# Optimization experiments

Measured on AMD Instinct MI355X. Metric: run time of the kernel, lower is better.

## Reference

```python
import jax, jax.numpy as jnp
import numpy as np
import math

NUM_HEADS = 8


def _dwconv(x, w, b, pad):
    # depthwise conv: x (B,C,H,W), w (C,1,k,k)
    c = x.shape[1]
    y = jax.lax.conv_general_dilated(
        x, w, window_strides=(1, 1), padding=[(pad, pad), (pad, pad)],
        feature_group_count=c, dimension_numbers=("NCHW", "OIHW", "NCHW"))
    return y + b[None, :, None, None]


def _conv(x, w, b, pad):
    y = jax.lax.conv_general_dilated(
        x, w, window_strides=(1, 1), padding=[(pad, pad), (pad, pad)],
        dimension_numbers=("NCHW", "OIHW", "NCHW"))
    return y + b[None, :, None, None]


def setup_inputs() -> dict:
    key = jax.random.key(0)
    ks = jax.random.split(key, 6)
    B, C, H, W = 8, 128, 128, 128
    x = jax.random.normal(ks[0], (B, C, H, W), dtype=jnp.float32)
    wq = jax.random.normal(ks[1], (C, 1, 9, 9), dtype=jnp.float32) * 0.05
    wk = jax.random.normal(ks[2], (C, 1, 9, 9), dtype=jnp.float32) * 0.05
    wv = jax.random.normal(ks[3], (C, 1, 9, 9), dtype=jnp.float32) * 0.05
    wo = jax.random.normal(ks[4], (C, C, 3, 3), dtype=jnp.float32) * 0.02
    bq = jnp.zeros((C,), jnp.float32)
    bk = jnp.zeros((C,), jnp.float32)
    bv = jnp.zeros((C,), jnp.float32)
    bo = jnp.zeros((C,), jnp.float32)
    return {"x": x, "wq": wq, "bq": bq, "wk": wk, "bk": bk,
            "wv": wv, "bv": bv, "wo": wo, "bo": bo}


def reference(x, wq, bq, wk, bk, wv, bv, wo, bo):
    b, c, h, w = x.shape
    hds = NUM_HEADS
    d = (h * w) // hds  # spatial dim split across heads
    q = _dwconv(x, wq, bq, 4).reshape(b, c, hds, d).transpose(0, 2, 1, 3)  # (b,hds,c,d)
    k = _dwconv(x, wk, bk, 4).reshape(b, c, hds, d).transpose(0, 2, 3, 1)  # (b,hds,d,c)
    v = _dwconv(x, wv, bv, 4).reshape(b, c, hds, d).transpose(0, 2, 1, 3)  # (b,hds,c,d)
    # channel attention: C x C scores per head, fp32 softmax
    qk = jnp.einsum("bhcd,bhde->bhce", q.astype(jnp.float32), k.astype(jnp.float32)) / math.sqrt(h * w)
    a = jnp.einsum("bhce,bhed->bhcd", jax.nn.softmax(qk, axis=-1), v.astype(jnp.float32))
    a = a.transpose(0, 2, 1, 3).reshape(b, c, h, w)
    return _conv(a, wo, bo, 1)
```

## Files before the change

### kernel.cpp

```cpp
#include <hip/hip_runtime.h>

#define BATCH 8
#define CH 128
#define HH 128
#define WW 128
#define HWSZ 16384
#define NHEADS 8
#define DHEAD 2048

typedef short bf16x8 __attribute__((ext_vector_type(8)));
typedef short bf16x4v __attribute__((ext_vector_type(4)));
typedef float f32x4 __attribute__((ext_vector_type(4)));
typedef float f32x2 __attribute__((ext_vector_type(2)));
typedef _Float16 f16x8 __attribute__((ext_vector_type(8)));
typedef _Float16 f16x4 __attribute__((ext_vector_type(4)));

static __device__ inline unsigned short f2bf(float f) {
    unsigned u = __builtin_bit_cast(unsigned, f);
    u += 0x7fff + ((u >> 16) & 1);
    return (unsigned short)(u >> 16);
}

__global__ __launch_bounds__(256) void toeplitz_prep_kernel(
    const float* __restrict__ wq, const float* __restrict__ wk,
    const float* __restrict__ wv, _Float16* __restrict__ Tp)
{
    const int g = blockIdx.x * 256 + threadIdx.x;
    const int c    = g / 1728;
    const int rem  = g - c * 1728;
    const int m    = rem >> 6;
    const int lane = rem & 63;
    const int conv = m / 9;
    const int dy   = m - conv * 9;
    const float* w = (conv == 0) ? wq : ((conv == 1) ? wk : wv);
    const int j    = lane & 15;
    const int kb   = (lane >> 4) << 3;
    f16x8 h;
    #pragma unroll
    for (int e = 0; e < 8; ++e) {
        const int d = kb + e - j;
        h[e] = (d >= 0 && d <= 8) ? (_Float16)w[c * 81 + dy * 9 + d]
                                  : (_Float16)0.f;
    }
    *(f16x8*)&Tp[(size_t)g * 8] = h;
}

__global__ __launch_bounds__(256) void dwconv_qkv_mfma_kernel(
    const float* __restrict__ x,
    const float* __restrict__ bq, const float* __restrict__ bk,
    const float* __restrict__ bv,
    const _Float16* __restrict__ Tp,
    unsigned short* __restrict__ Qb, unsigned short* __restrict__ Kb,
    unsigned short* __restrict__ Vb)
{
    const int bc = blockIdx.x;
    const int b  = bc >> 7;
    const int c  = bc & (CH - 1);

    __shared__ _Float16 img[136][144];

    const int tid  = threadIdx.x;
    const int wave = tid >> 6;
    const int lane = tid & 63;
    const int lx   = lane & 15;
    const int qd   = lane >> 4;

    f16x8 Btp[27];
    const _Float16* tp = Tp + (size_t)c * 13824 + (size_t)lane * 8;
    #pragma unroll
    for (int m = 0; m < 27; ++m)
        Btp[m] = *(const f16x8*)(tp + (size_t)m * 512);

    {
        f16x8 z = {0, 0, 0, 0, 0, 0, 0, 0};
        _Float16* flat = &img[0][0];
        for (int i = tid; i < 2448; i += 256)
            *(f16x8*)&flat[i * 8] = z;
    }
    __syncthreads();
    const float* xp = x + (size_t)bc * HWSZ;
    for (int i = tid; i < 4096; i += 256) {
        const float4 v = *(const float4*)&xp[i * 4];
        const int y  = i >> 5;
        const int xc = (i & 31) << 2;
        f16x4 h = {(_Float16)v.x, (_Float16)v.y, (_Float16)v.z, (_Float16)v.w};
        *(f16x4*)&img[y + 4][xc + 4] = h;
    }
    __syncthreads();

    const float bqv = bq[c], bkv = bk[c], bvv = bv[c];

    #pragma unroll 1
    for (int t = 0; t < 8; ++t) {
        const int sg = t * 4 + wave;
        const int yg = sg >> 2;
        const int y0 = yg << 4;
        const int x0 = (sg & 3) << 5;

        f32x4 aq0 = {bqv, bqv, bqv, bqv}, aq1 = aq0;
        f32x4 ak0 = {bkv, bkv, bkv, bkv}, ak1 = ak0;
        f32x4 av0 = {bvv, bvv, bvv, bvv}, av1 = av0;

        const _Float16* rp = &img[y0 + lx][x0 + (qd << 3)];
        #pragma unroll
        for (int dy = 0; dy < 9; ++dy) {
            const f16x8 a0 = *(const f16x8*)rp;
            const f16x8 a1 = *(const f16x8*)(rp + 16);
            rp += 144;
            aq0 = __builtin_amdgcn_mfma_f32_16x16x32_f16(a0, Btp[dy],      aq0, 0, 0, 0);
            aq1 = __builtin_amdgcn_mfma_f32_16x16x32_f16(a1, Btp[dy],      aq1, 0, 0, 0);
            ak0 = __builtin_amdgcn_mfma_f32_16x16x32_f16(a0, Btp[9 + dy],  ak0, 0, 0, 0);
            ak1 = __builtin_amdgcn_mfma_f32_16x16x32_f16(a1, Btp[9 + dy],  ak1, 0, 0, 0);
            av0 = __builtin_amdgcn_mfma_f32_16x16x32_f16(a0, Btp[18 + dy], av0, 0, 0, 0);
            av1 = __builtin_amdgcn_mfma_f32_16x16x32_f16(a1, Btp[18 + dy], av1, 0, 0, 0);
        }

        const size_t base = ((size_t)(b * 8 + yg) * CH + c) * DHEAD
                          + (size_t)(qd << 2) * WW + x0 + lx;
        #pragma unroll
        for (int r = 0; r < 4; ++r) {
            Qb[base + r * WW]      = f2bf(aq0[r]);
            Qb[base + r * WW + 16] = f2bf(aq1[r]);
            Kb[base + r * WW]      = f2bf(ak0[r]);
            Kb[base + r * WW + 16] = f2bf(ak1[r]);
            Vb[base + r * WW]      = f2bf(av0[r]);
            Vb[base + r * WW + 16] = f2bf(av1[r]);
        }
    }
}

__global__ __launch_bounds__(256) void qk_mfma_kernel(
    const unsigned short* __restrict__ Qb, const unsigned short* __restrict__ Kb,
    float* __restrict__ Spart)
{
    const int blk   = blockIdx.x;
    const int split = blk & 7;
    const int bh    = blk >> 3;
    const int t0    = split * 256;

    __shared__ unsigned short Qs[128][72];
    __shared__ unsigned short Ks[128][72];

    const int tid  = threadIdx.x;
    const int wave = tid >> 6;
    const int lane = tid & 63;
    const int lx   = lane & 15;
    const int qd   = lane >> 4;
    const int m0   = (wave & 1) * 64;
    const int n0   = (wave >> 1) * 64;

    f32x4 acc[4][4];
    #pragma unroll
    for (int mi = 0; mi < 4; ++mi)
        #pragma unroll
        for (int ni = 0; ni < 4; ++ni) acc[mi][ni] = (f32x4){0.f, 0.f, 0.f, 0.f};

    const unsigned short* Qp = Qb + (size_t)bh * CH * DHEAD;
    const unsigned short* Kp = Kb + (size_t)bh * CH * DHEAD;

    #pragma unroll 1
    for (int tc = 0; tc < 256; tc += 64) {
        __syncthreads();
        for (int i = tid; i < 1024; i += 256) {
            const int r  = i >> 3;
            const int cl = (i & 7) << 3;
            *(bf16x8*)&Qs[r][cl] = *(const bf16x8*)&Qp[(size_t)r * DHEAD + t0 + tc + cl];
            *(bf16x8*)&Ks[r][cl] = *(const bf16x8*)&Kp[(size_t)r * DHEAD + t0 + tc + cl];
        }
        __syncthreads();
        #pragma unroll
        for (int ki = 0; ki < 2; ++ki) {
            const int kc = ki * 32 + qd * 8;
            bf16x8 a[4], bv[4];
            #pragma unroll
            for (int mi = 0; mi < 4; ++mi)
                a[mi] = *(const bf16x8*)&Qs[m0 + mi * 16 + lx][kc];
            #pragma unroll
            for (int ni = 0; ni < 4; ++ni)
                bv[ni] = *(const bf16x8*)&Ks[n0 + ni * 16 + lx][kc];
            #pragma unroll
            for (int mi = 0; mi < 4; ++mi)
                #pragma unroll
                for (int ni = 0; ni < 4; ++ni)
                    acc[mi][ni] = __builtin_amdgcn_mfma_f32_16x16x32_bf16(
                        a[mi], bv[ni], acc[mi][ni], 0, 0, 0);
        }
    }
    float* Sp = Spart + ((size_t)split * 64 + bh) * (CH * CH);
    #pragma unroll
    for (int mi = 0; mi < 4; ++mi)
        #pragma unroll
        for (int r = 0; r < 4; ++r) {
            const int c = m0 + mi * 16 + qd * 4 + r;
            #pragma unroll
            for (int ni = 0; ni < 4; ++ni)
                Sp[c * CH + n0 + ni * 16 + lx] = acc[mi][ni][r];
        }
}

__global__ __launch_bounds__(256) void softmax_kernel(
    const float* __restrict__ Spart, unsigned short* __restrict__ Pb)
{
    const int row  = blockIdx.x * 4 + (threadIdx.x >> 6);
    const int lane = threadIdx.x & 63;
    float v0 = 0.f, v1 = 0.f;
    #pragma unroll
    for (int s = 0; s < 8; ++s) {
        const float* Sp = Spart + (size_t)s * 64 * CH * CH + (size_t)row * CH;
        v0 += Sp[lane];
        v1 += Sp[lane + 64];
    }
    v0 *= 0.0078125f; v1 *= 0.0078125f;
    float m = fmaxf(v0, v1);
    #pragma unroll
    for (int off = 32; off > 0; off >>= 1) m = fmaxf(m, __shfl_down(m, off));
    m = __shfl(m, 0);
    const float e0 = __expf(v0 - m);
    const float e1 = __expf(v1 - m);
    float s = e0 + e1;
    #pragma unroll
    for (int off = 32; off > 0; off >>= 1) s += __shfl_down(s, off);
    s = __shfl(s, 0);
    const float inv = 1.f / s;
    Pb[(size_t)row * CH + lane]      = f2bf(e0 * inv);
    Pb[(size_t)row * CH + lane + 64] = f2bf(e1 * inv);
}

__global__ __launch_bounds__(256) void pv_mfma_kernel(
    const unsigned short* __restrict__ Pb, const unsigned short* __restrict__ Vb,
    unsigned short* __restrict__ At)
{
    const int blk = blockIdx.x;
    const int t0  = (blk & 15) << 7;
    const int bh  = blk >> 4;

    __shared__ __align__(16) char smem[69632];
    unsigned short (*Ps)[136] = (unsigned short(*)[136])smem;
    unsigned short (*Vs)[136] = (unsigned short(*)[136])(smem + 34816);
    float (*So)[132] = (float(*)[132])smem;

    const int tid  = threadIdx.x;
    const int wave = tid >> 6;
    const int lane = tid & 63;
    const int lx   = lane & 15;
    const int qd   = lane >> 4;
    const int m0   = (wave & 1) * 64;
    const int n0   = (wave >> 1) * 64;

    const unsigned short* Pp = Pb + (size_t)bh * CH * CH;
    const unsigned short* Vp = Vb + (size_t)bh * CH * DHEAD;

    for (int i = tid; i < 2048; i += 256) {
        const int r  = i >> 4;
        const int cl = (i & 15) << 3;
        *(bf16x8*)&Ps[r][cl] = *(const bf16x8*)&Pp[(size_t)r * CH + cl];
    }
    for (int i = tid; i < 2048; i += 256) {
        const int e   = i & 127;
        const int tc8 = (i >> 7) << 3;
        const bf16x8 vv = *(const bf16x8*)&Vp[(size_t)e * DHEAD + t0 + tc8];
        #pragma unroll
        for (int j = 0; j < 8; ++j) Vs[tc8 + j][e] = (unsigned short)vv[j];
    }
    __syncthreads();

    f32x4 acc[4][4];
    #pragma unroll
    for (int mi = 0; mi < 4; ++mi)
        #pragma unroll
        for (int ni = 0; ni < 4; ++ni) acc[mi][ni] = (f32x4){0.f, 0.f, 0.f, 0.f};

    #pragma unroll
    for (int ki = 0; ki < 4; ++ki) {
        const int kc = ki * 32 + qd * 8;
        bf16x8 a[4], bv[4];
        #pragma unroll
        for (int mi = 0; mi < 4; ++mi)
            a[mi] = *(const bf16x8*)&Ps[m0 + mi * 16 + lx][kc];
        #pragma unroll
        for (int ni = 0; ni < 4; ++ni)
            bv[ni] = *(const bf16x8*)&Vs[n0 + ni * 16 + lx][kc];
        #pragma unroll
        for (int mi = 0; mi < 4; ++mi)
            #pragma unroll
            for (int ni = 0; ni < 4; ++ni)
                acc[mi][ni] = __builtin_amdgcn_mfma_f32_16x16x32_bf16(
                    a[mi], bv[ni], acc[mi][ni], 0, 0, 0);
    }

    __syncthreads();
    #pragma unroll
    for (int mi = 0; mi < 4; ++mi)
        #pragma unroll
        for (int ni = 0; ni < 4; ++ni)
            #pragma unroll
            for (int r = 0; r < 4; ++r)
                So[n0 + ni * 16 + lx][m0 + mi * 16 + qd * 4 + r] = acc[mi][ni][r];
    __syncthreads();

    const int t  = tid >> 1;
    const int ch = (tid & 1) * 64;
    const size_t orow = (((size_t)(bh >> 3) * HWSZ) + (size_t)(bh & 7) * DHEAD + t0 + t) * CH + ch;
    #pragma unroll
    for (int j = 0; j < 8; ++j) {
        const float4 f0 = *(const float4*)&So[t][ch + j * 8];
        const float4 f1 = *(const float4*)&So[t][ch + j * 8 + 4];
        bf16x8 h;
        h[0] = (short)f2bf(f0.x); h[1] = (short)f2bf(f0.y);
        h[2] = (short)f2bf(f0.z); h[3] = (short)f2bf(f0.w);
        h[4] = (short)f2bf(f1.x); h[5] = (short)f2bf(f1.y);
        h[6] = (short)f2bf(f1.z); h[7] = (short)f2bf(f1.w);
        *(bf16x8*)&At[orow + j * 8] = h;
    }
}

__global__ __launch_bounds__(256) void wprep_kernel(
    const float* __restrict__ wo, unsigned short* __restrict__ Wt)
{
    const int i = blockIdx.x * 256 + threadIdx.x;
    const int tap = i >> 14;
    const int rem = i & 16383;
    const int co  = rem >> 7;
    const int ci  = rem & 127;
    Wt[i] = f2bf(wo[(size_t)(co * CH + ci) * 9 + tap]);
}

__global__ __launch_bounds__(512, 2) void conv3x3_mfma_kernel(
    const unsigned short* __restrict__ At, const unsigned short* __restrict__ Wt,
    const float* __restrict__ bo, float* __restrict__ out)
{
    __shared__ __align__(16) char smem[149504];

    const int w    = ((blockIdx.x & 7) << 6) | (blockIdx.x >> 3);
    const int yp   = w & 63;
    const int b    = w >> 6;
    const int y0   = yp << 1;

    const int tid  = threadIdx.x;
    const int wave = tid >> 6;
    const int lane = tid & 63;
    const int lx   = lane & 15;
    const int qd   = lane >> 4;
    const int m0   = (wave & 1) << 6;
    const int n0   = (wave >> 1) << 6;
    const int rsel = n0 >> 7;
    const int xb   = n0 & 64;

    const int j0 = tid, j1 = tid + 512;
    const int co0 = j0 >> 3, cu0 = j0 & 7;
    const int co1 = j1 >> 3, cu1 = j1 & 7;
    const unsigned swo0 = (unsigned)((co0 * 128 + cu0 * 16) ^ ((co0 & 7) << 4)) + 133120u;
    const unsigned swo1 = (unsigned)((co1 * 128 + cu1 * 16) ^ ((co1 & 7) << 4)) + 133120u;

    float4 nwa = *(const float4*)&Wt[(size_t)co0 * 128 + cu0 * 8];
    float4 nwb = *(const float4*)&Wt[(size_t)co1 * 128 + cu1 * 8];

    const size_t abase = (size_t)b * HWSZ * CH;
    if (tid < 128) {
        const int r  = tid >> 5;
        const int cu = tid & 31;
        const int xp = (cu & 16) ? 129 : 0;
        const int u  = cu & 15;
        const unsigned off = (unsigned)(r * 33280 + xp * 256 + u * 16) ^ (((unsigned)xp & 7u) << 4);
        *(float4*)(smem + off) = make_float4(0.f, 0.f, 0.f, 0.f);
    }
    for (int i = tid; i < 8192; i += 512) {
        const int r   = i >> 11;
        const int rem = i & 2047;
        const int xx  = rem >> 4;
        const int u   = rem & 15;
        const int gy  = y0 - 1 + r;
        float4 v = make_float4(0.f, 0.f, 0.f, 0.f);
        if ((unsigned)gy < HH)
            v = *(const float4*)&At[abase + (size_t)gy * WW * CH + xx * CH + u * 8];
        const int xp = xx + 1;
        const unsigned off = (unsigned)(r * 33280 + xp * 256 + u * 16) ^ (((unsigned)xp & 7u) << 4);
        *(float4*)(smem + off) = v;
    }
    *(float4*)(smem + swo0) = nwa;
    *(float4*)(smem + swo1) = nwb;
    nwa = *(const float4*)&Wt[(size_t)co0 * 128 + 64 + cu0 * 8];
    nwb = *(const float4*)&Wt[(size_t)co1 * 128 + 64 + cu1 * 8];

    f32x4 acc[4][4];
    #pragma unroll
    for (int mi = 0; mi < 4; ++mi) {
        f32x4 bv;
        #pragma unroll
        for (int r = 0; r < 4; ++r) bv[r] = bo[m0 + mi * 16 + qd * 4 + r];
        #pragma unroll
        for (int ni = 0; ni < 4; ++ni) acc[mi][ni] = bv;
    }

    __syncthreads();

    #pragma unroll 1
    for (int s = 0; s < 18; ++s) {
        const int tap = s >> 1;
        const int dy  = (tap * 11) >> 5;
        const int txc = tap - dy * 3;
        const int kh  = s & 1;
        const int ra  = rsel + dy;

        #pragma unroll
        for (int ks = 0; ks < 2; ++ks) {
            const int wkb = ks * 64 + qd * 16;
            const int akb = kh * 128 + ks * 64 + qd * 16;
            bf16x8 a[4], bfr[4];
            #pragma unroll
            for (int mi = 0; mi < 4; ++mi) {
                const int co = m0 + mi * 16 + lx;
                a[mi] = *(const bf16x8*)(smem + 133120u +
                        (unsigned)((co * 128 + wkb) ^ ((co & 7) << 4)));
            }
            #pragma unroll
            for (int ni = 0; ni < 4; ++ni) {
                const int xp = xb + ni * 16 + lx + txc;
                const unsigned off = (unsigned)(ra * 33280 + xp * 256 + akb)
                                   ^ (((unsigned)xp & 7u) << 4);
                bfr[ni] = *(const bf16x8*)(smem + off);
            }
            #pragma unroll
            for (int mi = 0; mi < 4; ++mi)
                #pragma unroll
                for (int ni = 0; ni < 4; ++ni)
                    acc[mi][ni] = __builtin_amdgcn_mfma_f32_16x16x32_bf16(
                        a[mi], bfr[ni], acc[mi][ni], 0, 0, 0);
        }
        __syncthreads();
        if (s < 17) {
            *(float4*)(smem + swo0) = nwa;
            *(float4*)(smem + swo1) = nwb;
            if (s < 16) {
                const int s2 = s + 2;
                const size_t gb = (size_t)(s2 >> 1) * 16384 + (s2 & 1) * 64;
                nwa = *(const float4*)&Wt[gb + co0 * 128 + cu0 * 8];
                nwb = *(const float4*)&Wt[gb + co1 * 128 + cu1 * 8];
            }
            __syncthreads();
        }
    }

    const int gy = y0 + rsel;
    const size_t obase = (size_t)b * CH * HWSZ + (size_t)gy * WW + xb;
    #pragma unroll
    for (int mi = 0; mi < 4; ++mi) {
        #pragma unroll
        for (int r = 0; r < 4; ++r) {
            const int co = m0 + mi * 16 + qd * 4 + r;
            float* orow = out + obase + (size_t)co * HWSZ;
            #pragma unroll
            for (int ni = 0; ni < 4; ++ni)
                orow[ni * 16 + lx] = acc[mi][ni][r];
        }
    }
}

extern "C" void kernel_launch(void* const* d_in, const int* in_sizes, int n_in,
                              void* d_out, int out_size, void* d_ws, size_t ws_size,
                              hipStream_t stream)
{
    const float* x  = (const float*)d_in[0];
    const float* wq = (const float*)d_in[1];
    const float* bq = (const float*)d_in[2];
    const float* wk = (const float*)d_in[3];
    const float* bk = (const float*)d_in[4];
    const float* wv = (const float*)d_in[5];
    const float* bv = (const float*)d_in[6];
    const float* wo = (const float*)d_in[7];
    const float* bo = (const float*)d_in[8];

    char* ws = (char*)d_ws;
    unsigned short* Qb    = (unsigned short*)(ws);
    unsigned short* Kb    = (unsigned short*)(ws + (size_t)33554432);
    unsigned short* Vb    = (unsigned short*)(ws + (size_t)67108864);
    float*          Spart = (float*)        (ws + (size_t)100663296);
    unsigned short* Pb    = (unsigned short*)(ws + (size_t)134217728);
    unsigned short* At    = (unsigned short*)(ws + (size_t)136314880);
    unsigned short* Wt    = (unsigned short*)(ws + (size_t)169869312);
    _Float16*       Tp    = (_Float16*)      (ws + (size_t)100663296);

    toeplitz_prep_kernel<<<864, 256, 0, stream>>>(wq, wk, wv, Tp);
    dwconv_qkv_mfma_kernel<<<BATCH * CH, 256, 0, stream>>>(x, bq, bk, bv, Tp, Qb, Kb, Vb);
    wprep_kernel<<<576, 256, 0, stream>>>(wo, Wt);
    qk_mfma_kernel<<<64 * 8, 256, 0, stream>>>(Qb, Kb, Spart);
    softmax_kernel<<<2048, 256, 0, stream>>>(Spart, Pb);
    pv_mfma_kernel<<<64 * 16, 256, 0, stream>>>(Pb, Vb, At);
    conv3x3_mfma_kernel<<<BATCH * 64, 512, 0, stream>>>(At, Wt, bo, (float*)d_out);
}
```

Before: 268.9 us.

## Fuse QK and softmax, vectorize dwconv stores, double-buffer conv weights

Swaps the MFMA operand order in the depthwise conv so each lane holds four consecutive x outputs, which allows 8-byte vector stores in place of scalar bf16 stores. Replaces the split-K QK kernel plus separate softmax with one kernel: each block computes 32 full score rows over all of d and runs the softmax in shared memory. This drops the fp32 partial-score round trip and one launch, at the cost of fewer blocks (256) and a serial loop over d. The conv3x3 kernel double-buffers the weight tiles to remove one barrier per step and handles padding by zeroing operands in registers instead of keeping halo columns in shared memory, using a larger LDS allocation.

```diff
diff --git a/kernel.cpp b/kernel.cpp
--- a/kernel.cpp
+++ b/kernel.cpp
@@ -107,123 +107,157 @@
             const f16x8 a0 = *(const f16x8*)rp;
             const f16x8 a1 = *(const f16x8*)(rp + 16);
             rp += 144;
-            aq0 = __builtin_amdgcn_mfma_f32_16x16x32_f16(a0, Btp[dy],      aq0, 0, 0, 0);
-            aq1 = __builtin_amdgcn_mfma_f32_16x16x32_f16(a1, Btp[dy],      aq1, 0, 0, 0);
-            ak0 = __builtin_amdgcn_mfma_f32_16x16x32_f16(a0, Btp[9 + dy],  ak0, 0, 0, 0);
-            ak1 = __builtin_amdgcn_mfma_f32_16x16x32_f16(a1, Btp[9 + dy],  ak1, 0, 0, 0);
-            av0 = __builtin_amdgcn_mfma_f32_16x16x32_f16(a0, Btp[18 + dy], av0, 0, 0, 0);
-            av1 = __builtin_amdgcn_mfma_f32_16x16x32_f16(a1, Btp[18 + dy], av1, 0, 0, 0);
+            aq0 = __builtin_amdgcn_mfma_f32_16x16x32_f16(Btp[dy],      a0, aq0, 0, 0, 0);
+            aq1 = __builtin_amdgcn_mfma_f32_16x16x32_f16(Btp[dy],      a1, aq1, 0, 0, 0);
+            ak0 = __builtin_amdgcn_mfma_f32_16x16x32_f16(Btp[9 + dy],  a0, ak0, 0, 0, 0);
+            ak1 = __builtin_amdgcn_mfma_f32_16x16x32_f16(Btp[9 + dy],  a1, ak1, 0, 0, 0);
+            av0 = __builtin_amdgcn_mfma_f32_16x16x32_f16(Btp[18 + dy], a0, av0, 0, 0, 0);
+            av1 = __builtin_amdgcn_mfma_f32_16x16x32_f16(Btp[18 + dy], a1, av1, 0, 0, 0);
         }
 
         const size_t base = ((size_t)(b * 8 + yg) * CH + c) * DHEAD
-                          + (size_t)(qd << 2) * WW + x0 + lx;
-        #pragma unroll
-        for (int r = 0; r < 4; ++r) {
-            Qb[base + r * WW]      = f2bf(aq0[r]);
-            Qb[base + r * WW + 16] = f2bf(aq1[r]);
-            Kb[base + r * WW]      = f2bf(ak0[r]);
-            Kb[base + r * WW + 16] = f2bf(ak1[r]);
-            Vb[base + r * WW]      = f2bf(av0[r]);
-            Vb[base + r * WW + 16] = f2bf(av1[r]);
-        }
-    }
-}
-
-__global__ __launch_bounds__(256) void qk_mfma_kernel(
+                          + (size_t)lx * WW + x0 + (qd << 2);
+        bf16x4v h;
+        h[0] = (short)f2bf(aq0[0]); h[1] = (short)f2bf(aq0[1]);
+        h[2] = (short)f2bf(aq0[2]); h[3] = (short)f2bf(aq0[3]);
+        *(bf16x4v*)&Qb[base] = h;
+        h[0] = (short)f2bf(aq1[0]); h[1] = (short)f2bf(aq1[1]);
+        h[2] = (short)f2bf(aq1[2]); h[3] = (short)f2bf(aq1[3]);
+        *(bf16x4v*)&Qb[base + 16] = h;
+        h[0] = (short)f2bf(ak0[0]); h[1] = (short)f2bf(ak0[1]);
+        h[2] = (short)f2bf(ak0[2]); h[3] = (short)f2bf(ak0[3]);
+        *(bf16x4v*)&Kb[base] = h;
+        h[0] = (short)f2bf(ak1[0]); h[1] = (short)f2bf(ak1[1]);
+        h[2] = (short)f2bf(ak1[2]); h[3] = (short)f2bf(ak1[3]);
+        *(bf16x4v*)&Kb[base + 16] = h;
+        h[0] = (short)f2bf(av0[0]); h[1] = (short)f2bf(av0[1]);
+        h[2] = (short)f2bf(av0[2]); h[3] = (short)f2bf(av0[3]);
+        *(bf16x4v*)&Vb[base] = h;
+        h[0] = (short)f2bf(av1[0]); h[1] = (short)f2bf(av1[1]);
+        h[2] = (short)f2bf(av1[2]); h[3] = (short)f2bf(av1[3]);
+        *(bf16x4v*)&Vb[base + 16] = h;
+    }
+}
+
+__global__ __launch_bounds__(256) void qks_kernel(
     const unsigned short* __restrict__ Qb, const unsigned short* __restrict__ Kb,
-    float* __restrict__ Spart)
-{
-    const int blk   = blockIdx.x;
-    const int split = blk & 7;
-    const int bh    = blk >> 3;
-    const int t0    = split * 256;
-
-    __shared__ unsigned short Qs[128][72];
-    __shared__ unsigned short Ks[128][72];
+    unsigned short* __restrict__ Pb)
+{
+    const int blk = ((blockIdx.x & 7) << 5) | (blockIdx.x >> 3);
+    const int bh  = blk >> 2;
+    const int c0  = (blk & 3) << 5;
+
+    __shared__ __align__(16) char smem[41216];
 
     const int tid  = threadIdx.x;
     const int wave = tid >> 6;
     const int lane = tid & 63;
     const int lx   = lane & 15;
     const int qd   = lane >> 4;
-    const int m0   = (wave & 1) * 64;
-    const int n0   = (wave >> 1) * 64;
-
-    f32x4 acc[4][4];
-    #pragma unroll
-    for (int mi = 0; mi < 4; ++mi)
-        #pragma unroll
-        for (int ni = 0; ni < 4; ++ni) acc[mi][ni] = (f32x4){0.f, 0.f, 0.f, 0.f};
-
-    const unsigned short* Qp = Qb + (size_t)bh * CH * DHEAD;
+    const int n0   = wave << 5;
+
+    f32x4 acc[2][2];
+    #pragma unroll
+    for (int mi = 0; mi < 2; ++mi)
+        #pragma unroll
+        for (int ni = 0; ni < 2; ++ni) acc[mi][ni] = (f32x4){0.f, 0.f, 0.f, 0.f};
+
+    const unsigned short* Qp = Qb + ((size_t)bh * CH + c0) * DHEAD;
     const unsigned short* Kp = Kb + (size_t)bh * CH * DHEAD;
 
     #pragma unroll 1
-    for (int tc = 0; tc < 256; tc += 64) {
+    for (int chk = 0; chk < 16; ++chk) {
+        const int t0 = chk << 7;
         __syncthreads();
-        for (int i = tid; i < 1024; i += 256) {
-            const int r  = i >> 3;
-            const int cl = (i & 7) << 3;
-            *(bf16x8*)&Qs[r][cl] = *(const bf16x8*)&Qp[(size_t)r * DHEAD + t0 + tc + cl];
-            *(bf16x8*)&Ks[r][cl] = *(const bf16x8*)&Kp[(size_t)r * DHEAD + t0 + tc + cl];
+        for (int i = tid; i < 512; i += 256) {
+            const int r = i >> 4, u = i & 15;
+            const bf16x8 v = *(const bf16x8*)&Qp[(size_t)r * DHEAD + t0 + u * 8];
+            const unsigned off = (unsigned)((r << 8) + (u << 4)) ^ (((unsigned)r & 7u) << 4);
+            *(bf16x8*)(smem + off) = v;
+        }
+        for (int i = tid; i < 2048; i += 256) {
+            const int r = i >> 4, u = i & 15;
+            const bf16x8 v = *(const bf16x8*)&Kp[(size_t)r * DHEAD + t0 + u * 8];
+            const unsigned off = 8192u + ((unsigned)((r << 8) + (u << 4)) ^ (((unsigned)r & 7u) << 4));
+            *(bf16x8*)(smem + off) = v;
         }
         __syncthreads();
         #pragma unroll
-        for (int ki = 0; ki < 2; ++ki) {
+        for (int ki = 0; ki < 4; ++ki) {
             const int kc = ki * 32 + qd * 8;
-            bf16x8 a[4], bv[4];
-            #pragma unroll
-            for (int mi = 0; mi < 4; ++mi)
-                a[mi] = *(const bf16x8*)&Qs[m0 + mi * 16 + lx][kc];
-            #pragma unroll
-            for (int ni = 0; ni < 4; ++ni)
-                bv[ni] = *(const bf16x8*)&Ks[n0 + ni * 16 + lx][kc];
-            #pragma unroll
-            for (int mi = 0; mi < 4; ++mi)
+            bf16x8 a[2], bv[2];
+            #pragma unroll
+            for (int mi = 0; mi < 2; ++mi) {
+                const int r = mi * 16 + lx;
+                a[mi] = *(const bf16x8*)(smem +
+                        ((unsigned)((r << 8) + (kc << 1)) ^ (((unsigned)r & 7u) << 4)));
+            }
+            #pragma unroll
+            for (int ni = 0; ni < 2; ++ni) {
+                const int r = n0 + ni * 16 + lx;
+                bv[ni] = *(const bf16x8*)(smem + 8192u +
+                        ((unsigned)((r << 8) + (kc << 1)) ^ (((unsigned)r & 7u) << 4)));
+            }
+            #pragma unroll
+            for (int mi = 0; mi < 2; ++mi)
                 #pragma unroll
-                for (int ni = 0; ni < 4; ++ni)
+                for (int ni = 0; ni < 2; ++ni)
                     acc[mi][ni] = __builtin_amdgcn_mfma_f32_16x16x32_bf16(
                         a[mi], bv[ni], acc[mi][ni], 0, 0, 0);
         }
     }
-    float* Sp = Spart + ((size_t)split * 64 + bh) * (CH * CH);
-    #pragma unroll
-    for (int mi = 0; mi < 4; ++mi)
-        #pragma unroll
-        for (int r = 0; r < 4; ++r) {
-            const int c = m0 + mi * 16 + qd * 4 + r;
-            #pragma unroll
-            for (int ni = 0; ni < 4; ++ni)
-                Sp[c * CH + n0 + ni * 16 + lx] = acc[mi][ni][r];
-        }
-}
-
-__global__ __launch_bounds__(256) void softmax_kernel(
-    const float* __restrict__ Spart, unsigned short* __restrict__ Pb)
-{
-    const int row  = blockIdx.x * 4 + (threadIdx.x >> 6);
-    const int lane = threadIdx.x & 63;
-    float v0 = 0.f, v1 = 0.f;
-    #pragma unroll
-    for (int s = 0; s < 8; ++s) {
-        const float* Sp = Spart + (size_t)s * 64 * CH * CH + (size_t)row * CH;
-        v0 += Sp[lane];
-        v1 += Sp[lane + 64];
-    }
-    v0 *= 0.0078125f; v1 *= 0.0078125f;
-    float m = fmaxf(v0, v1);
-    #pragma unroll
-    for (int off = 32; off > 0; off >>= 1) m = fmaxf(m, __shfl_down(m, off));
-    m = __shfl(m, 0);
-    const float e0 = __expf(v0 - m);
-    const float e1 = __expf(v1 - m);
-    float s = e0 + e1;
-    #pragma unroll
-    for (int off = 32; off > 0; off >>= 1) s += __shfl_down(s, off);
-    s = __shfl(s, 0);
+
+    __syncthreads();
+    float* Ss = (float*)smem;
+    #pragma unroll
+    for (int mi = 0; mi < 2; ++mi)
+        #pragma unroll
+        for (int ni = 0; ni < 2; ++ni)
+            #pragma unroll
+            for (int r = 0; r < 4; ++r)
+                Ss[(mi * 16 + qd * 4 + r) * 132 + n0 + ni * 16 + lx] = acc[mi][ni][r];
+    __syncthreads();
+
+    const int rr   = tid >> 3;
+    const int col0 = (tid & 7) << 4;
+    f32x4 v0 = *(const f32x4*)&Ss[rr * 132 + col0];
+    f32x4 v1 = *(const f32x4*)&Ss[rr * 132 + col0 + 4];
+    f32x4 v2 = *(const f32x4*)&Ss[rr * 132 + col0 + 8];
+    f32x4 v3 = *(const f32x4*)&Ss[rr * 132 + col0 + 12];
+    const f32x4 sc = {0.0078125f, 0.0078125f, 0.0078125f, 0.0078125f};
+    v0 *= sc; v1 *= sc; v2 *= sc; v3 *= sc;
+    float m = v0[0];
+    #pragma unroll
+    for (int j = 1; j < 4; ++j) m = fmaxf(m, v0[j]);
+    #pragma unroll
+    for (int j = 0; j < 4; ++j) { m = fmaxf(m, v1[j]); m = fmaxf(m, v2[j]); m = fmaxf(m, v3[j]); }
+    m = fmaxf(m, __shfl_xor(m, 1));
+    m = fmaxf(m, __shfl_xor(m, 2));
+    m = fmaxf(m, __shfl_xor(m, 4));
+    float e[16];
+    #pragma unroll
+    for (int j = 0; j < 4; ++j) {
+        e[j]      = __expf(v0[j] - m);
+        e[4 + j]  = __expf(v1[j] - m);
+        e[8 + j]  = __expf(v2[j] - m);
+        e[12 + j] = __expf(v3[j] - m);
+    }
+    float s = 0.f;
+    #pragma unroll
+    for (int j = 0; j < 16; ++j) s += e[j];
+    s += __shfl_xor(s, 1);
+    s += __shfl_xor(s, 2);
+    s += __shfl_xor(s, 4);
     const float inv = 1.f / s;
-    Pb[(size_t)row * CH + lane]      = f2bf(e0 * inv);
-    Pb[(size_t)row * CH + lane + 64] = f2bf(e1 * inv);
+    bf16x8 h0, h1;
+    #pragma unroll
+    for (int j = 0; j < 8; ++j) {
+        h0[j] = (short)f2bf(e[j] * inv);
+        h1[j] = (short)f2bf(e[8 + j] * inv);
+    }
+    unsigned short* prow = Pb + ((size_t)bh * CH + c0 + rr) * CH + col0;
+    *(bf16x8*)&prow[0] = h0;
+    *(bf16x8*)&prow[8] = h1;
 }
 
 __global__ __launch_bounds__(256) void pv_mfma_kernel(
@@ -329,7 +363,7 @@
     const unsigned short* __restrict__ At, const unsigned short* __restrict__ Wt,
     const float* __restrict__ bo, float* __restrict__ out)
 {
-    __shared__ __align__(16) char smem[149504];
+    __shared__ __align__(16) char smem[163840];
 
     const int w    = ((blockIdx.x & 7) << 6) | (blockIdx.x >> 3);
     const int yp   = w & 63;
@@ -349,21 +383,13 @@
     const int j0 = tid, j1 = tid + 512;
     const int co0 = j0 >> 3, cu0 = j0 & 7;
     const int co1 = j1 >> 3, cu1 = j1 & 7;
-    const unsigned swo0 = (unsigned)((co0 * 128 + cu0 * 16) ^ ((co0 & 7) << 4)) + 133120u;
-    const unsigned swo1 = (unsigned)((co1 * 128 + cu1 * 16) ^ ((co1 & 7) << 4)) + 133120u;
+    const unsigned swo0 = (unsigned)((co0 * 128 + cu0 * 16) ^ ((co0 & 7) << 4)) + 131072u;
+    const unsigned swo1 = (unsigned)((co1 * 128 + cu1 * 16) ^ ((co1 & 7) << 4)) + 131072u;
 
     float4 nwa = *(const float4*)&Wt[(size_t)co0 * 128 + cu0 * 8];
     float4 nwb = *(const float4*)&Wt[(size_t)co1 * 128 + cu1 * 8];
 
     const size_t abase = (size_t)b * HWSZ * CH;
-    if (tid < 128) {
-        const int r  = tid >> 5;
-        const int cu = tid & 31;
-        const int xp = (cu & 16) ? 129 : 0;
-        const int u  = cu & 15;
-        const unsigned off = (unsigned)(r * 33280 + xp * 256 + u * 16) ^ (((unsigned)xp & 7u) << 4);
-        *(float4*)(smem + off) = make_float4(0.f, 0.f, 0.f, 0.f);
-    }
     for (int i = tid; i < 8192; i += 512) {
         const int r   = i >> 11;
         const int rem = i & 2047;
@@ -374,7 +400,8 @@
         if ((unsigned)gy < HH)
             v = *(const float4*)&At[abase + (size_t)gy * WW * CH + xx * CH + u * 8];
         const int xp = xx + 1;
-        const unsigned off = (unsigned)(r * 33280 + xp * 256 + u * 16) ^ (((unsigned)xp & 7u) << 4);
+        const unsigned off = (unsigned)((r << 15) + (xx << 8) + (u << 4))
+                           ^ (((unsigned)xp & 7u) << 4);
         *(float4*)(smem + off) = v;
     }
     *(float4*)(smem + swo0) = nwa;
@@ -401,6 +428,7 @@
         const int txc = tap - dy * 3;
         const int kh  = s & 1;
         const int ra  = rsel + dy;
+        const unsigned wbase = 131072u + (unsigned)(s & 1) * 16384u;
 
         #pragma unroll
         for (int ks = 0; ks < 2; ++ks) {
@@ -410,15 +438,18 @@
             #pragma unroll
             for (int mi = 0; mi < 4; ++mi) {
                 const int co = m0 + mi * 16 + lx;
-                a[mi] = *(const bf16x8*)(smem + 133120u +
+                a[mi] = *(const bf16x8*)(smem + wbase +
                         (unsigned)((co * 128 + wkb) ^ ((co & 7) << 4)));
             }
             #pragma unroll
             for (int ni = 0; ni < 4; ++ni) {
                 const int xp = xb + ni * 16 + lx + txc;
-                const unsigned off = (unsigned)(ra * 33280 + xp * 256 + akb)
-                                   ^ (((unsigned)xp & 7u) << 4);
+                const bool z = (unsigned)(xp - 1) >= 128u;
+                const int xpc = z ? 1 : xp;
+                const unsigned off = (unsigned)((ra << 15) + ((xpc - 1) << 8) + akb)
+                                   ^ (((unsigned)xpc & 7u) << 4);
                 bfr[ni] = *(const bf16x8*)(smem + off);
+                if (z) bfr[ni] = (bf16x8){0, 0, 0, 0, 0, 0, 0, 0};
             }
             #pragma unroll
             for (int mi = 0; mi < 4; ++mi)
@@ -427,18 +458,18 @@
                     acc[mi][ni] = __builtin_amdgcn_mfma_f32_16x16x32_bf16(
                         a[mi], bfr[ni], acc[mi][ni], 0, 0, 0);
         }
-        __syncthreads();
         if (s < 17) {
-            *(float4*)(smem + swo0) = nwa;
-            *(float4*)(smem + swo1) = nwb;
+            const unsigned nb = 131072u + (unsigned)((s + 1) & 1) * 16384u;
+            *(float4*)(smem + (swo0 - 131072u) + nb) = nwa;
+            *(float4*)(smem + (swo1 - 131072u) + nb) = nwb;
             if (s < 16) {
                 const int s2 = s + 2;
                 const size_t gb = (size_t)(s2 >> 1) * 16384 + (s2 & 1) * 64;
                 nwa = *(const float4*)&Wt[gb + co0 * 128 + cu0 * 8];
                 nwb = *(const float4*)&Wt[gb + co1 * 128 + cu1 * 8];
             }
-            __syncthreads();
-        }
+        }
+        __syncthreads();
     }
 
     const int gy = y0 + rsel;
@@ -474,7 +505,6 @@
     unsigned short* Qb    = (unsigned short*)(ws);
     unsigned short* Kb    = (unsigned short*)(ws + (size_t)33554432);
     unsigned short* Vb    = (unsigned short*)(ws + (size_t)67108864);
-    float*          Spart = (float*)        (ws + (size_t)100663296);
     unsigned short* Pb    = (unsigned short*)(ws + (size_t)134217728);
     unsigned short* At    = (unsigned short*)(ws + (size_t)136314880);
     unsigned short* Wt    = (unsigned short*)(ws + (size_t)169869312);
@@ -483,8 +513,7 @@
     toeplitz_prep_kernel<<<864, 256, 0, stream>>>(wq, wk, wv, Tp);
     dwconv_qkv_mfma_kernel<<<BATCH * CH, 256, 0, stream>>>(x, bq, bk, bv, Tp, Qb, Kb, Vb);
     wprep_kernel<<<576, 256, 0, stream>>>(wo, Wt);
-    qk_mfma_kernel<<<64 * 8, 256, 0, stream>>>(Qb, Kb, Spart);
-    softmax_kernel<<<2048, 256, 0, stream>>>(Spart, Pb);
+    qks_kernel<<<256, 256, 0, stream>>>(Qb, Kb, Pb);
     pv_mfma_kernel<<<64 * 16, 256, 0, stream>>>(Pb, Vb, At);
     conv3x3_mfma_kernel<<<BATCH * 64, 512, 0, stream>>>(At, Wt, bo, (float*)d_out);
 }
```

Measured after the change: 291.1 us. 8.3% more time.
